# Kernel optimization log

Measured on AMD Instinct MI355X. Metric: run time of the kernel, lower is better.

Reference implementation:

```python
import jax, jax.numpy as jnp
import numpy as np

# dims
B, S, H = 2, 256, 1024          # batch, global seq, global hidden
BH, NH = 384, 8                  # byte_hidden, num heads
HD = BH // NH                    # head dim = 48
P = 4                            # num_global_proj (seed byte positions)
S_C = 12                         # byte decode steps (= target.shape[2])
L = 4                            # num_byte_decoder_layers
V = 258                          # byte vocab (256 bytes + pad 256 + eos 257)
T = P + S_C
EOS = 257
SCALE = 1.0 / np.sqrt(HD)


def setup_inputs() -> dict:
    key = jax.random.key(0)
    ks = jax.random.split(key, 12)
    w = lambda k, shp: jax.random.normal(k, shp, jnp.float32) * 0.02
    return {
        "x": jax.random.normal(ks[0], (B, S, H), jnp.float32),
        "target": jax.random.randint(ks[1], (B, S, S_C), 0, V),
        "Wproj": w(ks[2], (H, P * BH)),
        "attn_norm": jnp.ones((L, BH), jnp.float32),
        "Wq": w(ks[3], (L, BH, BH)),
        "Wk": w(ks[4], (L, BH, BH)),
        "Wv": w(ks[5], (L, BH, BH)),
        "Wo": w(ks[6], (L, BH, BH)),
        "ffn_norm": jnp.ones((L, BH), jnp.float32),
        "W1": w(ks[7], (L, BH, 4 * BH)),
        "W2": w(ks[8], (L, 4 * BH, BH)),
        "Wlm": w(ks[9], (BH, V)),
    }


def _rms(x, g):
    return x * jax.lax.rsqrt(jnp.mean(x * x, -1, keepdims=True) + 1e-5) * g


def _block(x, kc, vc, pos, an, Wq, Wk, Wv, Wo, fn, W1, W2, causal):
    # x: [N, Lq, BH]; kc/vc: [N, T, NH, HD] KV caches; pos: static write offset
    N, Lq, _ = x.shape
    h = _rms(x, an)
    q = (h @ Wq).reshape(N, Lq, NH, HD)
    k = (h @ Wk).reshape(N, Lq, NH, HD)
    v = (h @ Wv).reshape(N, Lq, NH, HD)
    kc = jax.lax.dynamic_update_slice(kc, k, (0, pos, 0, 0))
    vc = jax.lax.dynamic_update_slice(vc, v, (0, pos, 0, 0))
    nk = pos + Lq
    sc = jnp.einsum('nqhd,nkhd->nhqk', q, kc[:, :nk]) * SCALE
    if causal:
        mask = jnp.arange(nk)[None, :] <= (pos + jnp.arange(Lq))[:, None]
        sc = jnp.where(mask[None, None], sc, jnp.float32(-1e30))
    p = jax.nn.softmax(sc, axis=-1)
    o = jnp.einsum('nhqk,nkhd->nqhd', p, vc[:, :nk]).reshape(N, Lq, BH)
    x = x + o @ Wo
    x = x + jax.nn.gelu(_rms(x, fn) @ W1, approximate=False) @ W2
    return x, kc, vc


def _forward(x, Wproj, attn_norm, Wq, Wk, Wv, Wo, ffn_norm, W1, W2, Wlm):
    N = B * S
    x0 = (x.reshape(N, H) @ Wproj).reshape(N, P, BH)
    x_out = jnp.zeros((N, T, BH), x0.dtype).at[:, :P].set(x0)
    kc = [jnp.zeros((N, T, NH, HD), x0.dtype) for _ in range(L)]
    vc = [jnp.zeros((N, T, NH, HD), x0.dtype) for _ in range(L)]
    finished = jnp.zeros((N,), bool)
    for i in range(S_C):
        if i == 0:
            pos, xi, causal = 0, x_out[:, :P], True          # prefill seed bytes
        else:
            pos, xi, causal = P + i - 1, x_out[:, P + i - 1:P + i], False  # decode 1 token
        for l in range(L):
            xi, kc[l], vc[l] = _block(xi, kc[l], vc[l], pos,
                                      attn_norm[l], Wq[l], Wk[l], Wv[l], Wo[l],
                                      ffn_norm[l], W1[l], W2[l], causal)
        gen = xi[:, -1]                                       # [N, BH]
        unf = ~finished
        # scatter only unfinished streams back (finished stay zero, as in torch)
        x_out = x_out.at[:, P + i].set(jnp.where(unf[:, None], gen, jnp.float32(0.0)))
        finished = finished | (unf & (jnp.argmax(gen, -1) == EOS))
    return x_out.reshape(B, S, T, BH)[:, :, P:, :] @ Wlm      # [B,S,S_C,V]


def reference(x, target, Wproj, attn_norm, Wq, Wk, Wv, Wo, ffn_norm, W1, W2, Wlm):
    del target  # only sets S_c (static here)
    return _forward(x, Wproj, attn_norm, Wq, Wk, Wv, Wo, ffn_norm, W1, W2, Wlm)
```

## Files before the change

### kernel.cpp

```cpp
#include <hip/hip_runtime.h>
#include <hip/hip_bf16.h>


constexpr int H_IN  = 1024;
constexpr int BH    = 384;
constexpr int NH    = 8;
constexpr int HD    = 48;
constexpr int PP    = 4;
constexpr int S_CNT = 12;
constexpr int NL    = 4;
constexpr int NV    = 258;
constexpr int TT    = 16;
constexpr int NSEQ  = 512;
constexpr int EOS_I = 257;
constexpr int NTH   = 768;
constexpr float RSCALE = 0.14433756729740646f;

typedef _Float16 h2 __attribute__((ext_vector_type(2)));
typedef _Float16 h8 __attribute__((ext_vector_type(8)));

union W16 { h8 v8; h2 h[4]; _Float16 e[8]; };

template<int N> struct IC { static constexpr int value = N; };

__device__ __forceinline__ float fdot2(h2 a, h2 b, float c) {
#if __has_builtin(__builtin_amdgcn_fdot2)
  return __builtin_amdgcn_fdot2(a, b, c, false);
#else
  return c + (float)a.x * (float)b.x + (float)a.y * (float)b.y;
#endif
}

__global__ __launch_bounds__(256)
void pack8_kernel(const float* __restrict__ src, const float* __restrict__ g,
                  h8* __restrict__ dst, int C, int stride3, int off3) {
  int c  = blockIdx.x * 256 + threadIdx.x;
  int j8 = blockIdx.y;
  if (c < C) {
    h8 v;
    #pragma unroll
    for (int r = 0; r < 8; r++) {
      int row = 8 * j8 + r;
      float s = g ? g[row] : 1.0f;
      v[r] = (_Float16)(src[(size_t)row * C + c] * s);
    }
    dst[((size_t)j8 * stride3 + off3) * C + c] = v;
  }
}

__global__ __launch_bounds__(NTH)
void decoder_kernel(const float* __restrict__ x,
                    const h8* __restrict__ Wproj8,
                    const h8* __restrict__ Wqkv8,
                    const h8* __restrict__ Wo8,
                    const h8* __restrict__ W18,
                    const h8* __restrict__ W28,
                    const h8* __restrict__ Wlm8,
                    float* __restrict__ out,
                    _Float16* __restrict__ kbuf,
                    _Float16* __restrict__ vbuf)
{
  __shared__ float xs[2][4][BH];
  __shared__ __align__(16) _Float16 xh[2][4][BH];
  __shared__ __align__(16) _Float16 qh[2][4][BH];
  __shared__ __align__(16) _Float16 oh[2][4][BH];
  __shared__ __align__(16) _Float16 k_cur[2][4][BH];
  __shared__ __align__(16) _Float16 v_cur[2][4][BH];
  __shared__ float sc[2][NH][4][TT];
  __shared__ __align__(16) union Scr {
    float qkvp[3][2][4][BH];
    float wop[2][4][BH];
    struct { __align__(16) _Float16 f1h[2][4][4*BH];
             float w2p[2][4][BH]; } ffn;
    __align__(16) _Float16 xin[2][H_IN];
  } scr;
  __shared__ float redsq[2][4][6];
  __shared__ float redv[12];
  __shared__ int   redi[12];
  __shared__ int   fin[2];

  const int tid = threadIdx.x;
  const int kg  = tid / BH;
  const int col = tid - kg * BH;
  const int sq  = kg;
  const int wid = tid >> 6;
  const int w6  = wid % 6;
  const int seq0 = blockIdx.x * 2;

  if (tid < 2) fin[tid] = 0;

  for (int s = 0; s < 2; s++) {
    const size_t base = (size_t)(seq0 + s) * H_IN;
    for (int j = tid; j < H_IN; j += NTH) scr.xin[s][j] = (_Float16)x[base + j];
  }
  __syncthreads();
  {
    float acc[2][2] = {};
    for (int j8 = 0; j8 < H_IN / 8; j8 += 4) {
      W16 w0[4], w1[4];
      #pragma unroll
      for (int u = 0; u < 4; u++) {
        w0[u].v8 = Wproj8[(size_t)(j8 + u) * (PP * BH) + tid];
        w1[u].v8 = Wproj8[(size_t)(j8 + u) * (PP * BH) + tid + NTH];
      }
      #pragma unroll
      for (int u = 0; u < 4; u++)
        #pragma unroll
        for (int s = 0; s < 2; s++) {
          W16 hv; hv.v8 = *(const h8*)&scr.xin[s][(j8 + u) * 8];
          #pragma unroll
          for (int r = 0; r < 4; r++) {
            acc[s][0] = fdot2(hv.h[r], w0[u].h[r], acc[s][0]);
            acc[s][1] = fdot2(hv.h[r], w1[u].h[r], acc[s][1]);
          }
        }
    }
    const int m0 = tid / BH, cc = tid - m0 * BH;
    #pragma unroll
    for (int s = 0; s < 2; s++) {
      xs[s][m0][cc]     = acc[s][0];  xh[s][m0][cc]     = (_Float16)acc[s][0];
      xs[s][m0 + 2][cc] = acc[s][1];  xh[s][m0 + 2][cc] = (_Float16)acc[s][1];
      float r0 = acc[s][0] * acc[s][0], r1 = acc[s][1] * acc[s][1];
      #pragma unroll
      for (int off = 32; off; off >>= 1) {
        r0 += __shfl_down(r0, off, 64); r1 += __shfl_down(r1, off, 64);
      }
      if ((tid & 63) == 0) { redsq[s][m0][w6] = r0; redsq[s][m0 + 2][w6] = r1; }
    }
  }
  __syncthreads();

  auto layers = [&](auto ntc, int pos, bool causal) {
    constexpr int NT = decltype(ntc)::value;
    const int nk = pos + NT;
    for (int l = 0; l < NL; l++) {
      {
        const size_t wb3 = ((size_t)(l * 48 + kg * 24) * 3) * BH + col;
        float aq[2][NT] = {}, ak[2][NT] = {}, av[2][NT] = {};
        for (int j8 = 0; j8 < 24; j8 += 4) {
          W16 wq[4], wk[4], wv[4];
          #pragma unroll
          for (int u = 0; u < 4; u++) {
            const size_t rb = wb3 + (size_t)(j8 + u) * 3 * BH;
            wq[u].v8 = Wqkv8[rb];
            wk[u].v8 = Wqkv8[rb + BH];
            wv[u].v8 = Wqkv8[rb + 2 * BH];
          }
          #pragma unroll
          for (int u = 0; u < 4; u++)
            #pragma unroll
            for (int s = 0; s < 2; s++)
              #pragma unroll
              for (int tok = 0; tok < NT; tok++) {
                W16 hv; hv.v8 = *(const h8*)&xh[s][tok][(kg * 24 + j8 + u) * 8];
                #pragma unroll
                for (int r = 0; r < 4; r++) {
                  aq[s][tok] = fdot2(hv.h[r], wq[u].h[r], aq[s][tok]);
                  ak[s][tok] = fdot2(hv.h[r], wk[u].h[r], ak[s][tok]);
                  av[s][tok] = fdot2(hv.h[r], wv[u].h[r], av[s][tok]);
                }
              }
        }
        {
          const int so = kg ^ 1;
          #pragma unroll
          for (int tok = 0; tok < NT; tok++) {
            scr.qkvp[0][so][tok][col] = aq[so][tok];
            scr.qkvp[1][so][tok][col] = ak[so][tok];
            scr.qkvp[2][so][tok][col] = av[so][tok];
          }
        }
        __syncthreads();
        {
          const int s = kg;
          const size_t cb = (((size_t)(seq0 + s) * NL + l) * TT + pos) * BH + col;
          #pragma unroll
          for (int tok = 0; tok < NT; tok++) {
            float ss = redsq[s][tok][0] + redsq[s][tok][1] + redsq[s][tok][2] +
                       redsq[s][tok][3] + redsq[s][tok][4] + redsq[s][tok][5];
            float sca = rsqrtf(ss * (1.0f / BH) + 1e-5f);
            float kv_ = (ak[s][tok] + scr.qkvp[1][s][tok][col]) * sca;
            float vv_ = (av[s][tok] + scr.qkvp[2][s][tok][col]) * sca;
            qh[s][tok][col] = (_Float16)((aq[s][tok] + scr.qkvp[0][s][tok][col]) * sca * RSCALE);
            k_cur[s][tok][col] = (_Float16)kv_;
            v_cur[s][tok][col] = (_Float16)vv_;
            kbuf[cb + (size_t)tok * BH] = (_Float16)kv_;
            vbuf[cb + (size_t)tok * BH] = (_Float16)vv_;
          }
        }
        __syncthreads();
      }
      if constexpr (NT == 1) {
        if (tid < 2 * NH * TT) {
          const int s = tid >> 7, r = tid & 127, h = r >> 4, j = r & 15;
          float d = -1e30f;
          if (j < nk) {
            const h8* kp8 = (j == pos)
                ? (const h8*)&k_cur[s][0][h * HD]
                : (const h8*)(kbuf + (((size_t)(seq0 + s) * NL + l) * TT + j) * BH + h * HD);
            d = 0.f;
            #pragma unroll
            for (int c6 = 0; c6 < 6; c6++) {
              W16 kk, qq;
              kk.v8 = kp8[c6];
              qq.v8 = *(const h8*)&qh[s][0][h * HD + c6 * 8];
              #pragma unroll
              for (int rr = 0; rr < 4; rr++) d = fdot2(qq.h[rr], kk.h[rr], d);
            }
          }
          float m = d;
          #pragma unroll
          for (int off = 8; off; off >>= 1) m = fmaxf(m, __shfl_xor(m, off, 16));
          float e = expf(d - m);
          float den = e;
          #pragma unroll
          for (int off = 8; off; off >>= 1) den += __shfl_xor(den, off, 16);
          sc[s][h][0][j] = e * (1.0f / den);
        }
        __syncthreads();
      } else {
        {
          const int nu = 2 * NH * NT * nk;
          if (tid < nu) {
            int s = tid / (NH * NT * nk), r = tid % (NH * NT * nk);
            int h = r / (NT * nk); int r2 = r % (NT * nk);
            int qi = r2 / nk, j = r2 % nk;
            float d;
            if (causal && j > pos + qi) d = -1e30f;
            else {
              d = 0.f;
              #pragma unroll
              for (int c6 = 0; c6 < 6; c6++) {
                W16 kk, qq;
                kk.v8 = *(const h8*)&k_cur[s][j][h * HD + c6 * 8];
                qq.v8 = *(const h8*)&qh[s][qi][h * HD + c6 * 8];
                #pragma unroll
                for (int rr = 0; rr < 4; rr++) d = fdot2(qq.h[rr], kk.h[rr], d);
              }
            }
            sc[s][h][qi][j] = d;
          }
        }
        __syncthreads();
        {
          const int nr = 2 * NH * NT;
          if (tid < nr) {
            int s = tid / (NH * NT), r = tid % (NH * NT);
            int h = r / NT, qi = r % NT;
            float m = -3.0e38f;
            for (int j = 0; j < nk; j++) m = fmaxf(m, sc[s][h][qi][j]);
            float den = 0.f;
            for (int j = 0; j < nk; j++) {
              float e = expf(sc[s][h][qi][j] - m);
              sc[s][h][qi][j] = e; den += e;
            }
            float inv = 1.0f / den;
            for (int j = 0; j < nk; j++) sc[s][h][qi][j] *= inv;
          }
        }
        __syncthreads();
      }
      {
        const size_t vb = (((size_t)(seq0 + sq) * NL + l) * TT) * BH + col;
        const int h = col / HD;
        #pragma unroll
        for (int tok = 0; tok < NT; tok++) {
          float acc = 0.f;
          if constexpr (NT == 1) {
            int j = 0;
            for (; j + 4 <= pos; j += 4) {
              float v0 = (float)vbuf[vb + (size_t)(j + 0) * BH];
              float v1 = (float)vbuf[vb + (size_t)(j + 1) * BH];
              float v2 = (float)vbuf[vb + (size_t)(j + 2) * BH];
              float v3 = (float)vbuf[vb + (size_t)(j + 3) * BH];
              acc += sc[sq][h][0][j] * v0 + sc[sq][h][0][j + 1] * v1 +
                     sc[sq][h][0][j + 2] * v2 + sc[sq][h][0][j + 3] * v3;
            }
            for (; j < pos; j++)
              acc += sc[sq][h][0][j] * (float)vbuf[vb + (size_t)j * BH];
            acc += sc[sq][h][0][pos] * (float)v_cur[sq][0][col];
          } else {
            #pragma unroll
            for (int j = 0; j < 4; j++)
              acc += sc[sq][h][tok][j] * (float)v_cur[sq][j][col];
          }
          oh[sq][tok][col] = (_Float16)acc;
        }
      }
      __syncthreads();
      {
        const size_t wb = ((size_t)l * 48 + kg * 24) * BH + col;
        float ao[2][NT] = {};
        for (int j8 = 0; j8 < 24; j8 += 8) {
          W16 w[8];
          #pragma unroll
          for (int u = 0; u < 8; u++) w[u].v8 = Wo8[wb + (size_t)(j8 + u) * BH];
          #pragma unroll
          for (int u = 0; u < 8; u++)
            #pragma unroll
            for (int s = 0; s < 2; s++)
              #pragma unroll
              for (int tok = 0; tok < NT; tok++) {
                W16 hv; hv.v8 = *(const h8*)&oh[s][tok][(kg * 24 + j8 + u) * 8];
                #pragma unroll
                for (int r = 0; r < 4; r++)
                  ao[s][tok] = fdot2(hv.h[r], w[u].h[r], ao[s][tok]);
              }
        }
        {
          const int so = kg ^ 1;
          #pragma unroll
          for (int tok = 0; tok < NT; tok++) scr.wop[so][tok][col] = ao[so][tok];
        }
        __syncthreads();
        {
          const int s = kg;
          #pragma unroll
          for (int tok = 0; tok < NT; tok++) {
            float xn = xs[s][tok][col] + ao[s][tok] + scr.wop[s][tok][col];
            xs[s][tok][col] = xn; xh[s][tok][col] = (_Float16)xn;
            float r = xn * xn;
            #pragma unroll
            for (int off = 32; off; off >>= 1) r += __shfl_down(r, off, 64);
            if ((tid & 63) == 0) redsq[s][tok][w6] = r;
          }
        }
        __syncthreads();
      }
      {
        float a1[2][NT][2] = {};
        for (int j8 = 0; j8 < 48; j8 += 4) {
          W16 w0[4], w1[4];
          #pragma unroll
          for (int u = 0; u < 4; u++) {
            w0[u].v8 = W18[((size_t)(l * 48 + j8 + u)) * (4 * BH) + tid];
            w1[u].v8 = W18[((size_t)(l * 48 + j8 + u)) * (4 * BH) + tid + NTH];
          }
          #pragma unroll
          for (int u = 0; u < 4; u++)
            #pragma unroll
            for (int s = 0; s < 2; s++)
              #pragma unroll
              for (int t = 0; t < NT; t++) {
                W16 hv; hv.v8 = *(const h8*)&xh[s][t][(j8 + u) * 8];
                #pragma unroll
                for (int r = 0; r < 4; r++) {
                  a1[s][t][0] = fdot2(hv.h[r], w0[u].h[r], a1[s][t][0]);
                  a1[s][t][1] = fdot2(hv.h[r], w1[u].h[r], a1[s][t][1]);
                }
              }
        }
        #pragma unroll
        for (int s = 0; s < 2; s++)
          #pragma unroll
          for (int t = 0; t < NT; t++) {
            float ss = redsq[s][t][0] + redsq[s][t][1] + redsq[s][t][2] +
                       redsq[s][t][3] + redsq[s][t][4] + redsq[s][t][5];
            float sca = rsqrtf(ss * (1.0f / BH) + 1e-5f);
            float z0 = a1[s][t][0] * sca, z1 = a1[s][t][1] * sca;
            scr.ffn.f1h[s][t][tid]       = (_Float16)(0.5f * z0 * (1.0f + erff(z0 * 0.7071067811865476f)));
            scr.ffn.f1h[s][t][tid + NTH] = (_Float16)(0.5f * z1 * (1.0f + erff(z1 * 0.7071067811865476f)));
          }
        __syncthreads();
        {
          float a2[2][NT] = {};
          for (int j8 = 0; j8 < 96; j8 += 8) {
            W16 w[8];
            #pragma unroll
            for (int u = 0; u < 8; u++)
              w[u].v8 = W28[((size_t)(l * 192 + kg * 96 + j8 + u)) * BH + col];
            #pragma unroll
            for (int u = 0; u < 8; u++)
              #pragma unroll
              for (int s = 0; s < 2; s++)
                #pragma unroll
                for (int t = 0; t < NT; t++) {
                  W16 fv; fv.v8 = *(const h8*)&scr.ffn.f1h[s][t][(kg * 96 + j8 + u) * 8];
                  #pragma unroll
                  for (int r = 0; r < 4; r++)
                    a2[s][t] = fdot2(fv.h[r], w[u].h[r], a2[s][t]);
                }
          }
          {
            const int so = kg ^ 1;
            #pragma unroll
            for (int t = 0; t < NT; t++) scr.ffn.w2p[so][t][col] = a2[so][t];
          }
          __syncthreads();
          {
            const int s = kg;
            #pragma unroll
            for (int t = 0; t < NT; t++) {
              float xn = xs[s][t][col] + a2[s][t] + scr.ffn.w2p[s][t][col];
              xs[s][t][col] = xn; xh[s][t][col] = (_Float16)xn;
              float r = xn * xn;
              #pragma unroll
              for (int off = 32; off; off >>= 1) r += __shfl_down(r, off, 64);
              if ((tid & 63) == 0) redsq[s][t][w6] = r;
              if (t == NT - 1 && l == NL - 1) {
                float v = xn; int idx = col;
                #pragma unroll
                for (int off = 32; off; off >>= 1) {
                  float v2 = __shfl_down(v, off, 64); int i2 = __shfl_down(idx, off, 64);
                  if (v2 > v || (v2 == v && i2 < idx)) { v = v2; idx = i2; }
                }
                if ((tid & 63) == 0) { redv[wid] = v; redi[wid] = idx; }
                float nxt = fin[s] ? 0.0f : xn;
                xs[s][0][col] = nxt; xh[s][0][col] = (_Float16)nxt;
                float rn = nxt * nxt;
                #pragma unroll
                for (int off = 32; off; off >>= 1) rn += __shfl_down(rn, off, 64);
                if ((tid & 63) == 0) redsq[s][0][w6] = rn;
              }
            }
          }
          __syncthreads();
        }
      }
    }
  };

  for (int i = 0; i < S_CNT; i++) {
    if (i == 0) layers(IC<4>{}, 0, true);
    else        layers(IC<1>{}, PP + i - 1, false);

    {
      if (col == 0) {
        const int b = sq * 6;
        float bv = redv[b]; int bi = redi[b];
        for (int w = 1; w < 6; w++)
          if (redv[b + w] > bv || (redv[b + w] == bv && redi[b + w] < bi)) {
            bv = redv[b + w]; bi = redi[b + w];
          }
        if (bi == EOS_I) fin[sq] = 1;
      }
      if (col < NV) {
        float acc = 0.f;
        for (int j8 = 0; j8 < 48; j8 += 8) {
          W16 w[8];
          #pragma unroll
          for (int u = 0; u < 8; u++) w[u].v8 = Wlm8[(size_t)(j8 + u) * NV + col];
          #pragma unroll
          for (int u = 0; u < 8; u++) {
            W16 gv; gv.v8 = *(const h8*)&xh[sq][0][(j8 + u) * 8];
            #pragma unroll
            for (int r = 0; r < 4; r++) acc = fdot2(gv.h[r], w[u].h[r], acc);
          }
        }
        out[((size_t)(seq0 + sq) * S_CNT + i) * NV + col] = acc;
      }
      __syncthreads();
    }
  }
}

extern "C" void kernel_launch(void* const* d_in, const int* in_sizes, int n_in,
                              void* d_out, int out_size, void* d_ws, size_t ws_size,
                              hipStream_t stream) {
  const float* x     = (const float*)d_in[0];
  const float* Wproj = (const float*)d_in[2];
  const float* an    = (const float*)d_in[3];
  const float* Wq    = (const float*)d_in[4];
  const float* Wk    = (const float*)d_in[5];
  const float* Wv    = (const float*)d_in[6];
  const float* Wo    = (const float*)d_in[7];
  const float* fn    = (const float*)d_in[8];
  const float* W1    = (const float*)d_in[9];
  const float* W2    = (const float*)d_in[10];
  const float* Wlm   = (const float*)d_in[11];
  float* out = (float*)d_out;
  (void)ws_size; (void)in_sizes; (void)n_in; (void)out_size;

  h8* w = (h8*)d_ws;
  const int n_proj = (H_IN / 8) * (PP * BH);
  const int n_qkv  = NL * (BH / 8) * BH * 3;
  const int n_qkvo = NL * (BH / 8) * BH;
  const int n_w1   = NL * (BH / 8) * (4 * BH);
  const int n_w2   = NL * (4 * BH / 8) * BH;
  const int n_lm   = (BH / 8) * NV;
  h8* Wproj_p = w;  w += n_proj;
  h8* Wqkv_p  = w;  w += n_qkv;
  h8* Wo_p    = w;  w += n_qkvo;
  h8* W1_p    = w;  w += n_w1;
  h8* W2_p    = w;  w += n_w2;
  h8* Wlm_p   = w;  w += n_lm;
  const size_t kv_elems = (size_t)NSEQ * NL * TT * BH;
  _Float16* kbuf = (_Float16*)w;
  _Float16* vbuf = kbuf + kv_elems;

  auto pack = [&](const float* src, const float* g, h8* dst, int R, int C,
                  int stride3, int off3) {
    dim3 grid((C + 255) / 256, R / 8);
    pack8_kernel<<<grid, 256, 0, stream>>>(src, g, dst, C, stride3, off3);
  };
  pack(Wproj, nullptr, Wproj_p, H_IN,        PP * BH, 1, 0);
  pack(Wq,    an,      Wqkv_p,  NL * BH,     BH,      3, 0);
  pack(Wk,    an,      Wqkv_p,  NL * BH,     BH,      3, 1);
  pack(Wv,    an,      Wqkv_p,  NL * BH,     BH,      3, 2);
  pack(Wo,    nullptr, Wo_p,    NL * BH,     BH,      1, 0);
  pack(W1,    fn,      W1_p,    NL * BH,     4 * BH,  1, 0);
  pack(W2,    nullptr, W2_p,    NL * 4 * BH, BH,      1, 0);
  pack(Wlm,   nullptr, Wlm_p,   BH,          NV,      1, 0);

  decoder_kernel<<<NSEQ / 2, NTH, 0, stream>>>(
      x, Wproj_p, Wqkv_p, Wo_p, W1_p, W2_p, Wlm_p, out, kbuf, vbuf);
}
```

Baseline: 2.341 ms.

## Assign each thread-half a full sequence instead of splitting K across halves

After: 3.408 ms. 1.46x slower.

```diff
diff --git a/kernel.cpp b/kernel.cpp
--- a/kernel.cpp
+++ b/kernel.cpp
@@ -68,10 +68,7 @@
   __shared__ __align__(16) _Float16 v_cur[2][4][BH];
   __shared__ float sc[2][NH][4][TT];
   __shared__ __align__(16) union Scr {
-    float qkvp[3][2][4][BH];
-    float wop[2][4][BH];
-    struct { __align__(16) _Float16 f1h[2][4][4*BH];
-             float w2p[2][4][BH]; } ffn;
+    __align__(16) _Float16 f1h[2][4][4*BH];
     __align__(16) _Float16 xin[2][H_IN];
   } scr;
   __shared__ float redsq[2][4][6];
@@ -80,9 +77,8 @@
   __shared__ int   fin[2];
 
   const int tid = threadIdx.x;
-  const int kg  = tid / BH;
-  const int col = tid - kg * BH;
-  const int sq  = kg;
+  const int sq  = tid / BH;
+  const int col = tid - sq * BH;
   const int wid = tid >> 6;
   const int w6  = wid % 6;
   const int seq0 = blockIdx.x * 2;
@@ -135,9 +131,9 @@
     const int nk = pos + NT;
     for (int l = 0; l < NL; l++) {
       {
-        const size_t wb3 = ((size_t)(l * 48 + kg * 24) * 3) * BH + col;
-        float aq[2][NT] = {}, ak[2][NT] = {}, av[2][NT] = {};
-        for (int j8 = 0; j8 < 24; j8 += 4) {
+        const size_t wb3 = ((size_t)(l * 48) * 3) * BH + col;
+        float aq[NT] = {}, ak[NT] = {}, av[NT] = {};
+        for (int j8 = 0; j8 < 48; j8 += 4) {
           W16 wq[4], wk[4], wv[4];
           #pragma unroll
           for (int u = 0; u < 4; u++) {
@@ -149,41 +145,28 @@
           #pragma unroll
           for (int u = 0; u < 4; u++)
             #pragma unroll
-            for (int s = 0; s < 2; s++)
-              #pragma unroll
-              for (int tok = 0; tok < NT; tok++) {
-                W16 hv; hv.v8 = *(const h8*)&xh[s][tok][(kg * 24 + j8 + u) * 8];
-                #pragma unroll
-                for (int r = 0; r < 4; r++) {
-                  aq[s][tok] = fdot2(hv.h[r], wq[u].h[r], aq[s][tok]);
-                  ak[s][tok] = fdot2(hv.h[r], wk[u].h[r], ak[s][tok]);
-                  av[s][tok] = fdot2(hv.h[r], wv[u].h[r], av[s][tok]);
-                }
+            for (int tok = 0; tok < NT; tok++) {
+              W16 hv; hv.v8 = *(const h8*)&xh[sq][tok][(j8 + u) * 8];
+              #pragma unroll
+              for (int r = 0; r < 4; r++) {
+                aq[tok] = fdot2(hv.h[r], wq[u].h[r], aq[tok]);
+                ak[tok] = fdot2(hv.h[r], wk[u].h[r], ak[tok]);
+                av[tok] = fdot2(hv.h[r], wv[u].h[r], av[tok]);
               }
+            }
         }
         {
-          const int so = kg ^ 1;
+          const size_t cb = (((size_t)(seq0 + sq) * NL + l) * TT + pos) * BH + col;
           #pragma unroll
           for (int tok = 0; tok < NT; tok++) {
-            scr.qkvp[0][so][tok][col] = aq[so][tok];
-            scr.qkvp[1][so][tok][col] = ak[so][tok];
-            scr.qkvp[2][so][tok][col] = av[so][tok];
-          }
-        }
-        __syncthreads();
-        {
-          const int s = kg;
-          const size_t cb = (((size_t)(seq0 + s) * NL + l) * TT + pos) * BH + col;
-          #pragma unroll
-          for (int tok = 0; tok < NT; tok++) {
-            float ss = redsq[s][tok][0] + redsq[s][tok][1] + redsq[s][tok][2] +
-                       redsq[s][tok][3] + redsq[s][tok][4] + redsq[s][tok][5];
+            float ss = redsq[sq][tok][0] + redsq[sq][tok][1] + redsq[sq][tok][2] +
+                       redsq[sq][tok][3] + redsq[sq][tok][4] + redsq[sq][tok][5];
             float sca = rsqrtf(ss * (1.0f / BH) + 1e-5f);
-            float kv_ = (ak[s][tok] + scr.qkvp[1][s][tok][col]) * sca;
-            float vv_ = (av[s][tok] + scr.qkvp[2][s][tok][col]) * sca;
-            qh[s][tok][col] = (_Float16)((aq[s][tok] + scr.qkvp[0][s][tok][col]) * sca * RSCALE);
-            k_cur[s][tok][col] = (_Float16)kv_;
-            v_cur[s][tok][col] = (_Float16)vv_;
+            float kv_ = ak[tok] * sca;
+            float vv_ = av[tok] * sca;
+            qh[sq][tok][col] = (_Float16)(aq[tok] * sca * RSCALE);
+            k_cur[sq][tok][col] = (_Float16)kv_;
+            v_cur[sq][tok][col] = (_Float16)vv_;
             kbuf[cb + (size_t)tok * BH] = (_Float16)kv_;
             vbuf[cb + (size_t)tok * BH] = (_Float16)vv_;
           }
@@ -289,114 +272,95 @@
       }
       __syncthreads();
       {
-        const size_t wb = ((size_t)l * 48 + kg * 24) * BH + col;
-        float ao[2][NT] = {};
-        for (int j8 = 0; j8 < 24; j8 += 8) {
+        const size_t wb = ((size_t)l * 48) * BH + col;
+        float ao[NT] = {};
+        for (int j8 = 0; j8 < 48; j8 += 8) {
           W16 w[8];
           #pragma unroll
           for (int u = 0; u < 8; u++) w[u].v8 = Wo8[wb + (size_t)(j8 + u) * BH];
           #pragma unroll
           for (int u = 0; u < 8; u++)
             #pragma unroll
-            for (int s = 0; s < 2; s++)
-              #pragma unroll
-              for (int tok = 0; tok < NT; tok++) {
-                W16 hv; hv.v8 = *(const h8*)&oh[s][tok][(kg * 24 + j8 + u) * 8];
+            for (int tok = 0; tok < NT; tok++) {
+              W16 hv; hv.v8 = *(const h8*)&oh[sq][tok][(j8 + u) * 8];
+              #pragma unroll
+              for (int r = 0; r < 4; r++)
+                ao[tok] = fdot2(hv.h[r], w[u].h[r], ao[tok]);
+            }
+        }
+        {
+          #pragma unroll
+          for (int tok = 0; tok < NT; tok++) {
+            float xn = xs[sq][tok][col] + ao[tok];
+            xs[sq][tok][col] = xn; xh[sq][tok][col] = (_Float16)xn;
+            float r = xn * xn;
+            #pragma unroll
+            for (int off = 32; off; off >>= 1) r += __shfl_down(r, off, 64);
+            if ((tid & 63) == 0) redsq[sq][tok][w6] = r;
+          }
+        }
+        __syncthreads();
+      }
+      {
+        float a1[NT][4] = {};
+        for (int j8 = 0; j8 < 48; j8 += 2) {
+          W16 wm[2][4];
+          #pragma unroll
+          for (int u = 0; u < 2; u++)
+            #pragma unroll
+            for (int m = 0; m < 4; m++)
+              wm[u][m].v8 = W18[((size_t)(l * 48 + j8 + u)) * (4 * BH) + col + m * BH];
+          #pragma unroll
+          for (int u = 0; u < 2; u++)
+            #pragma unroll
+            for (int t = 0; t < NT; t++) {
+              W16 hv; hv.v8 = *(const h8*)&xh[sq][t][(j8 + u) * 8];
+              #pragma unroll
+              for (int m = 0; m < 4; m++)
                 #pragma unroll
                 for (int r = 0; r < 4; r++)
-                  ao[s][tok] = fdot2(hv.h[r], w[u].h[r], ao[s][tok]);
+                  a1[t][m] = fdot2(hv.h[r], wm[u][m].h[r], a1[t][m]);
+            }
+        }
+        #pragma unroll
+        for (int t = 0; t < NT; t++) {
+          float ss = redsq[sq][t][0] + redsq[sq][t][1] + redsq[sq][t][2] +
+                     redsq[sq][t][3] + redsq[sq][t][4] + redsq[sq][t][5];
+          float sca = rsqrtf(ss * (1.0f / BH) + 1e-5f);
+          #pragma unroll
+          for (int m = 0; m < 4; m++) {
+            float z = a1[t][m] * sca;
+            scr.f1h[sq][t][col + m * BH] =
+                (_Float16)(0.5f * z * (1.0f + erff(z * 0.7071067811865476f)));
+          }
+        }
+        __syncthreads();
+        {
+          float a2[NT] = {};
+          for (int j8 = 0; j8 < 192; j8 += 8) {
+            W16 w[8];
+            #pragma unroll
+            for (int u = 0; u < 8; u++)
+              w[u].v8 = W28[((size_t)(l * 192 + j8 + u)) * BH + col];
+            #pragma unroll
+            for (int u = 0; u < 8; u++)
+              #pragma unroll
+              for (int t = 0; t < NT; t++) {
+                W16 fv; fv.v8 = *(const h8*)&scr.f1h[sq][t][(j8 + u) * 8];
+                #pragma unroll
+                for (int r = 0; r < 4; r++)
+                  a2[t] = fdot2(fv.h[r], w[u].h[r], a2[t]);
               }
-        }
-        {
-          const int so = kg ^ 1;
-          #pragma unroll
-          for (int tok = 0; tok < NT; tok++) scr.wop[so][tok][col] = ao[so][tok];
-        }
-        __syncthreads();
-        {
-          const int s = kg;
-          #pragma unroll
-          for (int tok = 0; tok < NT; tok++) {
-            float xn = xs[s][tok][col] + ao[s][tok] + scr.wop[s][tok][col];
-            xs[s][tok][col] = xn; xh[s][tok][col] = (_Float16)xn;
-            float r = xn * xn;
-            #pragma unroll
-            for (int off = 32; off; off >>= 1) r += __shfl_down(r, off, 64);
-            if ((tid & 63) == 0) redsq[s][tok][w6] = r;
-          }
-        }
-        __syncthreads();
-      }
-      {
-        float a1[2][NT][2] = {};
-        for (int j8 = 0; j8 < 48; j8 += 4) {
-          W16 w0[4], w1[4];
-          #pragma unroll
-          for (int u = 0; u < 4; u++) {
-            w0[u].v8 = W18[((size_t)(l * 48 + j8 + u)) * (4 * BH) + tid];
-            w1[u].v8 = W18[((size_t)(l * 48 + j8 + u)) * (4 * BH) + tid + NTH];
-          }
-          #pragma unroll
-          for (int u = 0; u < 4; u++)
-            #pragma unroll
-            for (int s = 0; s < 2; s++)
-              #pragma unroll
-              for (int t = 0; t < NT; t++) {
-                W16 hv; hv.v8 = *(const h8*)&xh[s][t][(j8 + u) * 8];
-                #pragma unroll
-                for (int r = 0; r < 4; r++) {
-                  a1[s][t][0] = fdot2(hv.h[r], w0[u].h[r], a1[s][t][0]);
-                  a1[s][t][1] = fdot2(hv.h[r], w1[u].h[r], a1[s][t][1]);
-                }
-              }
-        }
-        #pragma unroll
-        for (int s = 0; s < 2; s++)
-          #pragma unroll
-          for (int t = 0; t < NT; t++) {
-            float ss = redsq[s][t][0] + redsq[s][t][1] + redsq[s][t][2] +
-                       redsq[s][t][3] + redsq[s][t][4] + redsq[s][t][5];
-            float sca = rsqrtf(ss * (1.0f / BH) + 1e-5f);
-            float z0 = a1[s][t][0] * sca, z1 = a1[s][t][1] * sca;
-            scr.ffn.f1h[s][t][tid]       = (_Float16)(0.5f * z0 * (1.0f + erff(z0 * 0.7071067811865476f)));
-            scr.ffn.f1h[s][t][tid + NTH] = (_Float16)(0.5f * z1 * (1.0f + erff(z1 * 0.7071067811865476f)));
-          }
-        __syncthreads();
-        {
-          float a2[2][NT] = {};
-          for (int j8 = 0; j8 < 96; j8 += 8) {
-            W16 w[8];
-            #pragma unroll
-            for (int u = 0; u < 8; u++)
-              w[u].v8 = W28[((size_t)(l * 192 + kg * 96 + j8 + u)) * BH + col];
-            #pragma unroll
-            for (int u = 0; u < 8; u++)
-              #pragma unroll
-              for (int s = 0; s < 2; s++)
-                #pragma unroll
-                for (int t = 0; t < NT; t++) {
-                  W16 fv; fv.v8 = *(const h8*)&scr.ffn.f1h[s][t][(kg * 96 + j8 + u) * 8];
-                  #pragma unroll
-                  for (int r = 0; r < 4; r++)
-                    a2[s][t] = fdot2(fv.h[r], w[u].h[r], a2[s][t]);
-                }
           }
           {
-            const int so = kg ^ 1;
-            #pragma unroll
-            for (int t = 0; t < NT; t++) scr.ffn.w2p[so][t][col] = a2[so][t];
-          }
-          __syncthreads();
-          {
-            const int s = kg;
             #pragma unroll
             for (int t = 0; t < NT; t++) {
-              float xn = xs[s][t][col] + a2[s][t] + scr.ffn.w2p[s][t][col];
-              xs[s][t][col] = xn; xh[s][t][col] = (_Float16)xn;
+              float xn = xs[sq][t][col] + a2[t];
+              xs[sq][t][col] = xn; xh[sq][t][col] = (_Float16)xn;
               float r = xn * xn;
               #pragma unroll
               for (int off = 32; off; off >>= 1) r += __shfl_down(r, off, 64);
-              if ((tid & 63) == 0) redsq[s][t][w6] = r;
+              if ((tid & 63) == 0) redsq[sq][t][w6] = r;
               if (t == NT - 1 && l == NL - 1) {
                 float v = xn; int idx = col;
                 #pragma unroll
@@ -405,12 +369,12 @@
                   if (v2 > v || (v2 == v && i2 < idx)) { v = v2; idx = i2; }
                 }
                 if ((tid & 63) == 0) { redv[wid] = v; redi[wid] = idx; }
-                float nxt = fin[s] ? 0.0f : xn;
-                xs[s][0][col] = nxt; xh[s][0][col] = (_Float16)nxt;
+                float nxt = fin[sq] ? 0.0f : xn;
+                xs[sq][0][col] = nxt; xh[sq][0][col] = (_Float16)nxt;
                 float rn = nxt * nxt;
                 #pragma unroll
                 for (int off = 32; off; off >>= 1) rn += __shfl_down(rn, off, 64);
-                if ((tid & 63) == 0) redsq[s][0][w6] = rn;
+                if ((tid & 63) == 0) redsq[sq][0][w6] = rn;
               }
             }
           }
```

## Process four sequences per block to amortize weight loads across more streams

Applied to the files above, without the earlier changes.

After: 3.573 ms. 1.53x slower.

```diff
diff --git a/kernel.cpp b/kernel.cpp
--- a/kernel.cpp
+++ b/kernel.cpp
@@ -14,6 +14,7 @@
 constexpr int NSEQ  = 512;
 constexpr int EOS_I = 257;
 constexpr int NTH   = 768;
+constexpr int SPB   = 4;
 constexpr float RSCALE = 0.14433756729740646f;
 
 typedef _Float16 h2 __attribute__((ext_vector_type(2)));
@@ -60,42 +61,41 @@
                     _Float16* __restrict__ kbuf,
                     _Float16* __restrict__ vbuf)
 {
-  __shared__ float xs[2][4][BH];
-  __shared__ __align__(16) _Float16 xh[2][4][BH];
-  __shared__ __align__(16) _Float16 qh[2][4][BH];
-  __shared__ __align__(16) _Float16 oh[2][4][BH];
-  __shared__ __align__(16) _Float16 k_cur[2][4][BH];
-  __shared__ __align__(16) _Float16 v_cur[2][4][BH];
-  __shared__ float sc[2][NH][4][TT];
+  __shared__ float xs[SPB][4][BH];
+  __shared__ __align__(16) _Float16 xh[SPB][4][BH];
+  __shared__ __align__(16) _Float16 qh[SPB][4][BH];
+  __shared__ __align__(16) _Float16 oh[SPB][4][BH];
+  __shared__ __align__(16) _Float16 k_cur[SPB][4][BH];
+  __shared__ __align__(16) _Float16 v_cur[SPB][4][BH];
+  __shared__ float sc[SPB][NH][4][TT];
   __shared__ __align__(16) union Scr {
-    float qkvp[3][2][4][BH];
-    float wop[2][4][BH];
-    struct { __align__(16) _Float16 f1h[2][4][4*BH];
-             float w2p[2][4][BH]; } ffn;
-    __align__(16) _Float16 xin[2][H_IN];
+    float qkvp[3][8][BH];
+    float wop[8][BH];
+    struct { __align__(16) _Float16 f1h[SPB][4][4*BH];
+             float w2p[8][BH]; } ffn;
+    __align__(16) _Float16 xin[SPB][H_IN];
   } scr;
-  __shared__ float redsq[2][4][6];
-  __shared__ float redv[12];
-  __shared__ int   redi[12];
-  __shared__ int   fin[2];
+  __shared__ float redsq[SPB][4][6];
+  __shared__ float redv[SPB * 6];
+  __shared__ int   redi[SPB * 6];
+  __shared__ int   fin[SPB];
 
   const int tid = threadIdx.x;
   const int kg  = tid / BH;
   const int col = tid - kg * BH;
-  const int sq  = kg;
   const int wid = tid >> 6;
   const int w6  = wid % 6;
-  const int seq0 = blockIdx.x * 2;
-
-  if (tid < 2) fin[tid] = 0;
-
-  for (int s = 0; s < 2; s++) {
+  const int seq0 = blockIdx.x * SPB;
+
+  if (tid < SPB) fin[tid] = 0;
+
+  for (int s = 0; s < SPB; s++) {
     const size_t base = (size_t)(seq0 + s) * H_IN;
     for (int j = tid; j < H_IN; j += NTH) scr.xin[s][j] = (_Float16)x[base + j];
   }
   __syncthreads();
   {
-    float acc[2][2] = {};
+    float acc[SPB][2] = {};
     for (int j8 = 0; j8 < H_IN / 8; j8 += 4) {
       W16 w0[4], w1[4];
       #pragma unroll
@@ -106,7 +106,7 @@
       #pragma unroll
       for (int u = 0; u < 4; u++)
         #pragma unroll
-        for (int s = 0; s < 2; s++) {
+        for (int s = 0; s < SPB; s++) {
           W16 hv; hv.v8 = *(const h8*)&scr.xin[s][(j8 + u) * 8];
           #pragma unroll
           for (int r = 0; r < 4; r++) {
@@ -117,7 +117,7 @@
     }
     const int m0 = tid / BH, cc = tid - m0 * BH;
     #pragma unroll
-    for (int s = 0; s < 2; s++) {
+    for (int s = 0; s < SPB; s++) {
       xs[s][m0][cc]     = acc[s][0];  xh[s][m0][cc]     = (_Float16)acc[s][0];
       xs[s][m0 + 2][cc] = acc[s][1];  xh[s][m0 + 2][cc] = (_Float16)acc[s][1];
       float r0 = acc[s][0] * acc[s][0], r1 = acc[s][1] * acc[s][1];
@@ -130,13 +130,15 @@
   }
   __syncthreads();
 
-  auto layers = [&](auto ntc, int pos, bool causal) {
+  auto layers = [&](auto ntc, auto sbc, int base, int pos, bool causal) {
     constexpr int NT = decltype(ntc)::value;
+    constexpr int SB = decltype(sbc)::value;
+    constexpr int HB = SB / 2;
     const int nk = pos + NT;
     for (int l = 0; l < NL; l++) {
       {
         const size_t wb3 = ((size_t)(l * 48 + kg * 24) * 3) * BH + col;
-        float aq[2][NT] = {}, ak[2][NT] = {}, av[2][NT] = {};
+        float aq[SB][NT] = {}, ak[SB][NT] = {}, av[SB][NT] = {};
         for (int j8 = 0; j8 < 24; j8 += 4) {
           W16 wq[4], wk[4], wv[4];
           #pragma unroll
@@ -149,10 +151,10 @@
           #pragma unroll
           for (int u = 0; u < 4; u++)
             #pragma unroll
-            for (int s = 0; s < 2; s++)
+            for (int s = 0; s < SB; s++)
               #pragma unroll
               for (int tok = 0; tok < NT; tok++) {
-                W16 hv; hv.v8 = *(const h8*)&xh[s][tok][(kg * 24 + j8 + u) * 8];
+                W16 hv; hv.v8 = *(const h8*)&xh[base + s][tok][(kg * 24 + j8 + u) * 8];
                 #pragma unroll
                 for (int r = 0; r < 4; r++) {
                   aq[s][tok] = fdot2(hv.h[r], wq[u].h[r], aq[s][tok]);
@@ -162,36 +164,43 @@
               }
         }
         {
-          const int so = kg ^ 1;
-          #pragma unroll
-          for (int tok = 0; tok < NT; tok++) {
-            scr.qkvp[0][so][tok][col] = aq[so][tok];
-            scr.qkvp[1][so][tok][col] = ak[so][tok];
-            scr.qkvp[2][so][tok][col] = av[so][tok];
-          }
-        }
-        __syncthreads();
-        {
-          const int s = kg;
-          const size_t cb = (((size_t)(seq0 + s) * NL + l) * TT + pos) * BH + col;
-          #pragma unroll
-          for (int tok = 0; tok < NT; tok++) {
-            float ss = redsq[s][tok][0] + redsq[s][tok][1] + redsq[s][tok][2] +
-                       redsq[s][tok][3] + redsq[s][tok][4] + redsq[s][tok][5];
-            float sca = rsqrtf(ss * (1.0f / BH) + 1e-5f);
-            float kv_ = (ak[s][tok] + scr.qkvp[1][s][tok][col]) * sca;
-            float vv_ = (av[s][tok] + scr.qkvp[2][s][tok][col]) * sca;
-            qh[s][tok][col] = (_Float16)((aq[s][tok] + scr.qkvp[0][s][tok][col]) * sca * RSCALE);
-            k_cur[s][tok][col] = (_Float16)kv_;
-            v_cur[s][tok][col] = (_Float16)vv_;
-            kbuf[cb + (size_t)tok * BH] = (_Float16)kv_;
-            vbuf[cb + (size_t)tok * BH] = (_Float16)vv_;
+          #pragma unroll
+          for (int s2 = 0; s2 < HB; s2++) {
+            const int ls = (kg ^ 1) * HB + s2;
+            #pragma unroll
+            for (int tok = 0; tok < NT; tok++) {
+              scr.qkvp[0][ls * NT + tok][col] = aq[ls][tok];
+              scr.qkvp[1][ls * NT + tok][col] = ak[ls][tok];
+              scr.qkvp[2][ls * NT + tok][col] = av[ls][tok];
+            }
+          }
+        }
+        __syncthreads();
+        {
+          #pragma unroll
+          for (int s2 = 0; s2 < HB; s2++) {
+            const int ls = kg * HB + s2;
+            const int gs = base + ls;
+            const size_t cb = (((size_t)(seq0 + gs) * NL + l) * TT + pos) * BH + col;
+            #pragma unroll
+            for (int tok = 0; tok < NT; tok++) {
+              float ss = redsq[gs][tok][0] + redsq[gs][tok][1] + redsq[gs][tok][2] +
+                         redsq[gs][tok][3] + redsq[gs][tok][4] + redsq[gs][tok][5];
+              float sca = rsqrtf(ss * (1.0f / BH) + 1e-5f);
+              float kv_ = (ak[ls][tok] + scr.qkvp[1][ls * NT + tok][col]) * sca;
+              float vv_ = (av[ls][tok] + scr.qkvp[2][ls * NT + tok][col]) * sca;
+              qh[gs][tok][col] = (_Float16)((aq[ls][tok] + scr.qkvp[0][ls * NT + tok][col]) * sca * RSCALE);
+              k_cur[gs][tok][col] = (_Float16)kv_;
+              v_cur[gs][tok][col] = (_Float16)vv_;
+              kbuf[cb + (size_t)tok * BH] = (_Float16)kv_;
+              vbuf[cb + (size_t)tok * BH] = (_Float16)vv_;
+            }
           }
         }
         __syncthreads();
       }
       if constexpr (NT == 1) {
-        if (tid < 2 * NH * TT) {
+        if (tid < SPB * NH * TT) {
           const int s = tid >> 7, r = tid & 127, h = r >> 4, j = r & 15;
           float d = -1e30f;
           if (j < nk) {
@@ -220,11 +229,12 @@
         __syncthreads();
       } else {
         {
-          const int nu = 2 * NH * NT * nk;
+          const int nu = SB * NH * NT * nk;
           if (tid < nu) {
             int s = tid / (NH * NT * nk), r = tid % (NH * NT * nk);
             int h = r / (NT * nk); int r2 = r % (NT * nk);
             int qi = r2 / nk, j = r2 % nk;
+            const int gs = base + s;
             float d;
             if (causal && j > pos + qi) d = -1e30f;
             else {
@@ -232,65 +242,70 @@
               #pragma unroll
               for (int c6 = 0; c6 < 6; c6++) {
                 W16 kk, qq;
-                kk.v8 = *(const h8*)&k_cur[s][j][h * HD + c6 * 8];
-                qq.v8 = *(const h8*)&qh[s][qi][h * HD + c6 * 8];
+                kk.v8 = *(const h8*)&k_cur[gs][j][h * HD + c6 * 8];
+                qq.v8 = *(const h8*)&qh[gs][qi][h * HD + c6 * 8];
                 #pragma unroll
                 for (int rr = 0; rr < 4; rr++) d = fdot2(qq.h[rr], kk.h[rr], d);
               }
             }
-            sc[s][h][qi][j] = d;
-          }
-        }
-        __syncthreads();
-        {
-          const int nr = 2 * NH * NT;
+            sc[gs][h][qi][j] = d;
+          }
+        }
+        __syncthreads();
+        {
+          const int nr = SB * NH * NT;
           if (tid < nr) {
             int s = tid / (NH * NT), r = tid % (NH * NT);
             int h = r / NT, qi = r % NT;
+            const int gs = base + s;
             float m = -3.0e38f;
-            for (int j = 0; j < nk; j++) m = fmaxf(m, sc[s][h][qi][j]);
+            for (int j = 0; j < nk; j++) m = fmaxf(m, sc[gs][h][qi][j]);
             float den = 0.f;
             for (int j = 0; j < nk; j++) {
-              float e = expf(sc[s][h][qi][j] - m);
-              sc[s][h][qi][j] = e; den += e;
+              float e = expf(sc[gs][h][qi][j] - m);
+              sc[gs][h][qi][j] = e; den += e;
             }
             float inv = 1.0f / den;
-            for (int j = 0; j < nk; j++) sc[s][h][qi][j] *= inv;
+            for (int j = 0; j < nk; j++) sc[gs][h][qi][j] *= inv;
           }
         }
         __syncthreads();
       }
       {
-        const size_t vb = (((size_t)(seq0 + sq) * NL + l) * TT) * BH + col;
         const int h = col / HD;
         #pragma unroll
-        for (int tok = 0; tok < NT; tok++) {
-          float acc = 0.f;
-          if constexpr (NT == 1) {
-            int j = 0;
-            for (; j + 4 <= pos; j += 4) {
-              float v0 = (float)vbuf[vb + (size_t)(j + 0) * BH];
-              float v1 = (float)vbuf[vb + (size_t)(j + 1) * BH];
-              float v2 = (float)vbuf[vb + (size_t)(j + 2) * BH];
-              float v3 = (float)vbuf[vb + (size_t)(j + 3) * BH];
-              acc += sc[sq][h][0][j] * v0 + sc[sq][h][0][j + 1] * v1 +
-                     sc[sq][h][0][j + 2] * v2 + sc[sq][h][0][j + 3] * v3;
-            }
-            for (; j < pos; j++)
-              acc += sc[sq][h][0][j] * (float)vbuf[vb + (size_t)j * BH];
-            acc += sc[sq][h][0][pos] * (float)v_cur[sq][0][col];
-          } else {
-            #pragma unroll
-            for (int j = 0; j < 4; j++)
-              acc += sc[sq][h][tok][j] * (float)v_cur[sq][j][col];
-          }
-          oh[sq][tok][col] = (_Float16)acc;
+        for (int s2 = 0; s2 < HB; s2++) {
+          const int gs = base + kg * HB + s2;
+          const size_t vb = (((size_t)(seq0 + gs) * NL + l) * TT) * BH + col;
+          #pragma unroll
+          for (int tok = 0; tok < NT; tok++) {
+            float acc = 0.f;
+            if constexpr (NT == 1) {
+              int j = 0;
+              for (; j + 4 <= pos; j += 4) {
+                float v0 = (float)vbuf[vb + (size_t)(j + 0) * BH];
+                float v1 = (float)vbuf[vb + (size_t)(j + 1) * BH];
+                float v2 = (float)vbuf[vb + (size_t)(j + 2) * BH];
+                float v3 = (float)vbuf[vb + (size_t)(j + 3) * BH];
+                acc += sc[gs][h][0][j] * v0 + sc[gs][h][0][j + 1] * v1 +
+                       sc[gs][h][0][j + 2] * v2 + sc[gs][h][0][j + 3] * v3;
+              }
+              for (; j < pos; j++)
+                acc += sc[gs][h][0][j] * (float)vbuf[vb + (size_t)j * BH];
+              acc += sc[gs][h][0][pos] * (float)v_cur[gs][0][col];
+            } else {
+              #pragma unroll
+              for (int j = 0; j < 4; j++)
+                acc += sc[gs][h][tok][j] * (float)v_cur[gs][j][col];
+            }
+            oh[gs][tok][col] = (_Float16)acc;
+          }
         }
       }
       __syncthreads();
       {
         const size_t wb = ((size_t)l * 48 + kg * 24) * BH + col;
-        float ao[2][NT] = {};
+        float ao[SB][NT] = {};
         for (int j8 = 0; j8 < 24; j8 += 8) {
           W16 w[8];
           #pragma unroll
@@ -298,37 +313,45 @@
           #pragma unroll
           for (int u = 0; u < 8; u++)
             #pragma unroll
-            for (int s = 0; s < 2; s++)
+            for (int s = 0; s < SB; s++)
               #pragma unroll
               for (int tok = 0; tok < NT; tok++) {
-                W16 hv; hv.v8 = *(const h8*)&oh[s][tok][(kg * 24 + j8 + u) * 8];
+                W16 hv; hv.v8 = *(const h8*)&oh[base + s][tok][(kg * 24 + j8 + u) * 8];
                 #pragma unroll
                 for (int r = 0; r < 4; r++)
                   ao[s][tok] = fdot2(hv.h[r], w[u].h[r], ao[s][tok]);
               }
         }
         {
-          const int so = kg ^ 1;
-          #pragma unroll
-          for (int tok = 0; tok < NT; tok++) scr.wop[so][tok][col] = ao[so][tok];
-        }
-        __syncthreads();
-        {
-          const int s = kg;
-          #pragma unroll
-          for (int tok = 0; tok < NT; tok++) {
-            float xn = xs[s][tok][col] + ao[s][tok] + scr.wop[s][tok][col];
-            xs[s][tok][col] = xn; xh[s][tok][col] = (_Float16)xn;
-            float r = xn * xn;
-            #pragma unroll
-            for (int off = 32; off; off >>= 1) r += __shfl_down(r, off, 64);
-            if ((tid & 63) == 0) redsq[s][tok][w6] = r;
+          #pragma unroll
+          for (int s2 = 0; s2 < HB; s2++) {
+            const int ls = (kg ^ 1) * HB + s2;
+            #pragma unroll
+            for (int tok = 0; tok < NT; tok++)
+              scr.wop[ls * NT + tok][col] = ao[ls][tok];
+          }
+        }
+        __syncthreads();
+        {
+          #pragma unroll
+          for (int s2 = 0; s2 < HB; s2++) {
+            const int ls = kg * HB + s2;
+            const int gs = base + ls;
+            #pragma unroll
+            for (int tok = 0; tok < NT; tok++) {
+              float xn = xs[gs][tok][col] + ao[ls][tok] + scr.wop[ls * NT + tok][col];
+              xs[gs][tok][col] = xn; xh[gs][tok][col] = (_Float16)xn;
+              float r = xn * xn;
+              #pragma unroll
+              for (int off = 32; off; off >>= 1) r += __shfl_down(r, off, 64);
+              if ((tid & 63) == 0) redsq[gs][tok][w6] = r;
+            }
           }
         }
         __syncthreads();
       }
       {
-        float a1[2][NT][2] = {};
+        float a1[SB][NT][2] = {};
         for (int j8 = 0; j8 < 48; j8 += 4) {
           W16 w0[4], w1[4];
           #pragma unroll
@@ -339,10 +362,10 @@
           #pragma unroll
           for (int u = 0; u < 4; u++)
             #pragma unroll
-            for (int s = 0; s < 2; s++)
+            for (int s = 0; s < SB; s++)
               #pragma unroll
               for (int t = 0; t < NT; t++) {
-                W16 hv; hv.v8 = *(const h8*)&xh[s][t][(j8 + u) * 8];
+                W16 hv; hv.v8 = *(const h8*)&xh[base + s][t][(j8 + u) * 8];
                 #pragma unroll
                 for (int r = 0; r < 4; r++) {
                   a1[s][t][0] = fdot2(hv.h[r], w0[u].h[r], a1[s][t][0]);
@@ -351,19 +374,20 @@
               }
         }
         #pragma unroll
-        for (int s = 0; s < 2; s++)
+        for (int s = 0; s < SB; s++)
           #pragma unroll
           for (int t = 0; t < NT; t++) {
-            float ss = redsq[s][t][0] + redsq[s][t][1] + redsq[s][t][2] +
-                       redsq[s][t][3] + redsq[s][t][4] + redsq[s][t][5];
+            const int gs = base + s;
+            float ss = redsq[gs][t][0] + redsq[gs][t][1] + redsq[gs][t][2] +
+                       redsq[gs][t][3] + redsq[gs][t][4] + redsq[gs][t][5];
             float sca = rsqrtf(ss * (1.0f / BH) + 1e-5f);
             float z0 = a1[s][t][0] * sca, z1 = a1[s][t][1] * sca;
-            scr.ffn.f1h[s][t][tid]       = (_Float16)(0.5f * z0 * (1.0f + erff(z0 * 0.7071067811865476f)));
-            scr.ffn.f1h[s][t][tid + NTH] = (_Float16)(0.5f * z1 * (1.0f + erff(z1 * 0.7071067811865476f)));
-          }
-        __syncthreads();
-        {
-          float a2[2][NT] = {};
+            scr.ffn.f1h[gs][t][tid]       = (_Float16)(0.5f * z0 * (1.0f + erff(z0 * 0.7071067811865476f)));
+            scr.ffn.f1h[gs][t][tid + NTH] = (_Float16)(0.5f * z1 * (1.0f + erff(z1 * 0.7071067811865476f)));
+          }
+        __syncthreads();
+        {
+          float a2[SB][NT] = {};
           for (int j8 = 0; j8 < 96; j8 += 8) {
             W16 w[8];
             #pragma unroll
@@ -372,45 +396,53 @@
             #pragma unroll
             for (int u = 0; u < 8; u++)
               #pragma unroll
-              for (int s = 0; s < 2; s++)
+              for (int s = 0; s < SB; s++)
                 #pragma unroll
                 for (int t = 0; t < NT; t++) {
-                  W16 fv; fv.v8 = *(const h8*)&scr.ffn.f1h[s][t][(kg * 96 + j8 + u) * 8];
+                  W16 fv; fv.v8 = *(const h8*)&scr.ffn.f1h[base + s][t][(kg * 96 + j8 + u) * 8];
                   #pragma unroll
                   for (int r = 0; r < 4; r++)
                     a2[s][t] = fdot2(fv.h[r], w[u].h[r], a2[s][t]);
                 }
           }
           {
-            const int so = kg ^ 1;
-            #pragma unroll
-            for (int t = 0; t < NT; t++) scr.ffn.w2p[so][t][col] = a2[so][t];
+            #pragma unroll
+            for (int s2 = 0; s2 < HB; s2++) {
+              const int ls = (kg ^ 1) * HB + s2;
+              #pragma unroll
+              for (int t = 0; t < NT; t++)
+                scr.ffn.w2p[ls * NT + t][col] = a2[ls][t];
+            }
           }
           __syncthreads();
           {
-            const int s = kg;
-            #pragma unroll
-            for (int t = 0; t < NT; t++) {
-              float xn = xs[s][t][col] + a2[s][t] + scr.ffn.w2p[s][t][col];
-              xs[s][t][col] = xn; xh[s][t][col] = (_Float16)xn;
-              float r = xn * xn;
-              #pragma unroll
-              for (int off = 32; off; off >>= 1) r += __shfl_down(r, off, 64);
-              if ((tid & 63) == 0) redsq[s][t][w6] = r;
-              if (t == NT - 1 && l == NL - 1) {
-                float v = xn; int idx = col;
+            #pragma unroll
+            for (int s2 = 0; s2 < HB; s2++) {
+              const int ls = kg * HB + s2;
+              const int gs = base + ls;
+              #pragma unroll
+              for (int t = 0; t < NT; t++) {
+                float xn = xs[gs][t][col] + a2[ls][t] + scr.ffn.w2p[ls * NT + t][col];
+                xs[gs][t][col] = xn; xh[gs][t][col] = (_Float16)xn;
+                float r = xn * xn;
                 #pragma unroll
-                for (int off = 32; off; off >>= 1) {
-                  float v2 = __shfl_down(v, off, 64); int i2 = __shfl_down(idx, off, 64);
-                  if (v2 > v || (v2 == v && i2 < idx)) { v = v2; idx = i2; }
+                for (int off = 32; off; off >>= 1) r += __shfl_down(r, off, 64);
+                if ((tid & 63) == 0) redsq[gs][t][w6] = r;
+                if (t == NT - 1 && l == NL - 1) {
+                  float v = xn; int idx = col;
+                  #pragma unroll
+                  for (int off = 32; off; off >>= 1) {
+                    float v2 = __shfl_down(v, off, 64); int i2 = __shfl_down(idx, off, 64);
+                    if (v2 > v || (v2 == v && i2 < idx)) { v = v2; idx = i2; }
+                  }
+                  if ((tid & 63) == 0) { redv[gs * 6 + w6] = v; redi[gs * 6 + w6] = idx; }
+                  float nxt = fin[gs] ? 0.0f : xn;
+                  xs[gs][0][col] = nxt; xh[gs][0][col] = (_Float16)nxt;
+                  float rn = nxt * nxt;
+                  #pragma unroll
+                  for (int off = 32; off; off >>= 1) rn += __shfl_down(rn, off, 64);
+                  if ((tid & 63) == 0) redsq[gs][0][w6] = rn;
                 }
-                if ((tid & 63) == 0) { redv[wid] = v; redi[wid] = idx; }
-                float nxt = fin[s] ? 0.0f : xn;
-                xs[s][0][col] = nxt; xh[s][0][col] = (_Float16)nxt;
-                float rn = nxt * nxt;
-                #pragma unroll
-                for (int off = 32; off; off >>= 1) rn += __shfl_down(rn, off, 64);
-                if ((tid & 63) == 0) redsq[s][0][w6] = rn;
               }
             }
           }
@@ -421,33 +453,45 @@
   };
 
   for (int i = 0; i < S_CNT; i++) {
-    if (i == 0) layers(IC<4>{}, 0, true);
-    else        layers(IC<1>{}, PP + i - 1, false);
+    if (i == 0) {
+      layers(IC<4>{}, IC<2>{}, 0, 0, true);
+      layers(IC<4>{}, IC<2>{}, 2, 0, true);
+    } else {
+      layers(IC<1>{}, IC<4>{}, 0, PP + i - 1, false);
+    }
 
     {
       if (col == 0) {
-        const int b = sq * 6;
-        float bv = redv[b]; int bi = redi[b];
-        for (int w = 1; w < 6; w++)
-          if (redv[b + w] > bv || (redv[b + w] == bv && redi[b + w] < bi)) {
-            bv = redv[b + w]; bi = redi[b + w];
-          }
-        if (bi == EOS_I) fin[sq] = 1;
+        #pragma unroll
+        for (int s2 = 0; s2 < 2; s2++) {
+          const int gs = kg * 2 + s2;
+          const int b = gs * 6;
+          float bv = redv[b]; int bi = redi[b];
+          for (int w = 1; w < 6; w++)
+            if (redv[b + w] > bv || (redv[b + w] == bv && redi[b + w] < bi)) {
+              bv = redv[b + w]; bi = redi[b + w];
+            }
+          if (bi == EOS_I) fin[gs] = 1;
+        }
       }
       if (col < NV) {
-        float acc = 0.f;
+        float acc[2] = {};
         for (int j8 = 0; j8 < 48; j8 += 8) {
           W16 w[8];
           #pragma unroll
           for (int u = 0; u < 8; u++) w[u].v8 = Wlm8[(size_t)(j8 + u) * NV + col];
           #pragma unroll
-          for (int u = 0; u < 8; u++) {
-            W16 gv; gv.v8 = *(const h8*)&xh[sq][0][(j8 + u) * 8];
-            #pragma unroll
-            for (int r = 0; r < 4; r++) acc = fdot2(gv.h[r], w[u].h[r], acc);
-          }
-        }
-        out[((size_t)(seq0 + sq) * S_CNT + i) * NV + col] = acc;
+          for (int u = 0; u < 8; u++)
+            #pragma unroll
+            for (int s2 = 0; s2 < 2; s2++) {
+              W16 gv; gv.v8 = *(const h8*)&xh[kg * 2 + s2][0][(j8 + u) * 8];
+              #pragma unroll
+              for (int r = 0; r < 4; r++) acc[s2] = fdot2(gv.h[r], w[u].h[r], acc[s2]);
+            }
+        }
+        #pragma unroll
+        for (int s2 = 0; s2 < 2; s2++)
+          out[((size_t)(seq0 + kg * 2 + s2) * S_CNT + i) * NV + col] = acc[s2];
       }
       __syncthreads();
     }
@@ -502,6 +546,6 @@
   pack(W2,    nullptr, W2_p,    NL * 4 * BH, BH,      1, 0);
   pack(Wlm,   nullptr, Wlm_p,   BH,          NV,      1, 0);
 
-  decoder_kernel<<<NSEQ / 2, NTH, 0, stream>>>(
+  decoder_kernel<<<NSEQ / SPB, NTH, 0, stream>>>(
       x, Wproj_p, Wqkv_p, Wo_p, W1_p, W2_p, Wlm_p, out, kbuf, vbuf);
 }
```
